# Kernel tuning notes

Measured on AMD Instinct MI355X. Metric: run time of the kernel, lower is better.

## Reference

```python
import jax, jax.numpy as jnp
import numpy as np

N = 100000
D = 128
E = 3200000

def setup_inputs() -> dict:
    key = jax.random.key(0)
    k1, k2, k3 = jax.random.split(key, 3)
    mu = jax.random.normal(k1, (N, D), dtype=jnp.float32)
    log_sigma = jax.random.normal(k2, (N, D), dtype=jnp.float32)
    edge_index = jax.random.randint(k3, (2, E), 0, N, dtype=jnp.int64)
    return {"mu": mu, "log_sigma": log_sigma, "edge_index": edge_index}

def reference(mu, log_sigma, edge_index):
    # elbo() for variational_distribution='Gaussian'
    sigma = jnp.exp(log_sigma)
    # likelihood: gather endpoints, squared L2 distance, log(sigmoid(-d2))
    diff = mu[edge_index[0]] - mu[edge_index[1]]        # [E, D]
    d2 = jnp.sum(diff * diff, axis=1)                    # [E]
    log_likelihood = jnp.sum(jax.nn.log_sigmoid(-d2))    # log(sigmoid(-d2)), stable
    # Gaussian KL to standard normal prior
    kl = 0.5 * jnp.sum(sigma * sigma + mu * mu - log_sigma - 1.0)
    return -log_likelihood + kl
```

## Files before the change

### kernel.cpp

```cpp
#include <hip/hip_runtime.h>


#define NN 100000
#define DD 128
#define NBI 8
#define NBJ 16
#define NBINS 128
#define BSI 12500
#define BSJ 6250

#define NKL 512
#define NSCA 1024
#define SLICEA 32u
#define CAPA 32768u
#define OCAP 131072u
#define LOVF 768
#define SENT 0xFFFFFFFFu

#define QSCALE 21.166666f
#define S2Q    0.0022320293f

#define CAPB 26624u
#define NKLB 512
#define NSCB 1536

typedef unsigned int uint_t;
typedef float floatx2 __attribute__((ext_vector_type(2)));

#define WA_OCURS  64
#define WA_OFLOW  1024
#define WA_MU8    (WA_OFLOW + 1048576)
#define WA_PAIRS  (WA_MU8 + 12800000)
#define WA_END    (WA_PAIRS + 16777216)

#define WB_CURSOR 256
#define WB_MU8    16384
#define WB_PAIRS  (WB_MU8 + 12800000)
#define PAIRB_BYTES (NBINS * (int)CAPB * 4)
#define WB_END    (WB_PAIRS + PAIRB_BYTES)

__device__ inline double block_reduce_add(double v) {
    for (int off = 32; off > 0; off >>= 1)
        v += __shfl_down(v, off, 64);
    __shared__ double lds[8];
    int wid  = threadIdx.x >> 6;
    int lane = threadIdx.x & 63;
    if (lane == 0) lds[wid] = v;
    __syncthreads();
    double r = 0.0;
    if (threadIdx.x == 0) {
        int nw = (blockDim.x + 63) >> 6;
        for (int w = 0; w < nw; ++w) r += lds[w];
    }
    return r;
}

__device__ inline double edge_term(float d2) {
    double t = (double)d2;
    if (d2 < 30.0f) t += (double)log1pf(expf(-d2));
    return t;
}

__device__ inline float d2_fp32(const float* __restrict__ mu, int i, int j) {
    const float* pa = mu + (size_t)i * DD;
    const float* pb = mu + (size_t)j * DD;
    float d2 = 0.0f;
    for (int d = 0; d < DD; ++d) {
        float df = pa[d] - pb[d];
        d2 += df * df;
    }
    return d2;
}

__device__ inline int dot4acc(unsigned int a, unsigned int b, int acc) {
#if __has_builtin(__builtin_amdgcn_sdot4)
    return __builtin_amdgcn_sdot4((int)a, (int)b, acc, false);
#else
    int s = acc;
    #pragma unroll
    for (int t = 0; t < 4; ++t) {
        int xa = (int)((a >> (8 * t)) & 0xFFu); xa = (xa ^ 0x80) - 0x80;
        int xb = (int)((b >> (8 * t)) & 0xFFu); xb = (xb ^ 0x80) - 0x80;
        s += xa * xb;
    }
    return s;
#endif
}

__device__ inline int d2_int_part(uint4 a, uint4 b) {
    int daa = 0, dbb = 0, dab = 0;
    daa = dot4acc(a.x, a.x, daa); daa = dot4acc(a.y, a.y, daa);
    daa = dot4acc(a.z, a.z, daa); daa = dot4acc(a.w, a.w, daa);
    dbb = dot4acc(b.x, b.x, dbb); dbb = dot4acc(b.y, b.y, dbb);
    dbb = dot4acc(b.z, b.z, dbb); dbb = dot4acc(b.w, b.w, dbb);
    dab = dot4acc(a.x, b.x, dab); dab = dot4acc(a.y, b.y, dab);
    dab = dot4acc(a.z, b.z, dab); dab = dot4acc(a.w, b.w, dab);
    return daa + dbb - 2 * dab;
}

__device__ inline float d2_part(uint4 a, uint4 b) {
    float p = 0.0f;
    const unsigned int* pa = &a.x;
    const unsigned int* pb = &b.x;
    #pragma unroll
    for (int k = 0; k < 4; ++k) {
        floatx2 a0 = __builtin_amdgcn_cvt_pk_f32_fp8(pa[k], false);
        floatx2 a1 = __builtin_amdgcn_cvt_pk_f32_fp8(pa[k], true);
        floatx2 b0 = __builtin_amdgcn_cvt_pk_f32_fp8(pb[k], false);
        floatx2 b1 = __builtin_amdgcn_cvt_pk_f32_fp8(pb[k], true);
        float d0 = a0.x - b0.x;
        float d1 = a0.y - b0.y;
        float d2 = a1.x - b1.x;
        float d3 = a1.y - b1.y;
        p += d0 * d0 + d1 * d1 + d2 * d2 + d3 * d3;
    }
    return p;
}

__global__ void front_kernel(const float* __restrict__ mu,
                             const float* __restrict__ ls,
                             unsigned int* __restrict__ mu8,
                             const int* __restrict__ ei,
                             uint_t* __restrict__ pairs,
                             uint2* __restrict__ oflow,
                             uint_t* __restrict__ ocurs,
                             double* __restrict__ ws,
                             int total4, int E, int chunk) {
    __shared__ uint_t lcnt[NBINS];
    __shared__ uint_t stage[NBINS * (int)SLICEA];
    __shared__ uint2  lovf[LOVF];
    __shared__ uint_t lovfc;
    __shared__ uint_t obase;
    double acc = 0.0;
    if (blockIdx.x < NKL) {
        int stride = NKL * blockDim.x;
        for (int i = blockIdx.x * blockDim.x + threadIdx.x; i < total4; i += stride) {
            float4 m = reinterpret_cast<const float4*>(mu)[i];
            float4 s = reinterpret_cast<const float4*>(ls)[i];
            float v;
            v  = 0.5f * (expf(2.0f * s.x) + m.x * m.x - s.x - 1.0f);
            v += 0.5f * (expf(2.0f * s.y) + m.y * m.y - s.y - 1.0f);
            v += 0.5f * (expf(2.0f * s.z) + m.z * m.z - s.z - 1.0f);
            v += 0.5f * (expf(2.0f * s.w) + m.w * m.w - s.w - 1.0f);
            acc += (double)v;
            int q0 = __float2int_rn(fminf(fmaxf(m.x * QSCALE, -127.f), 127.f));
            int q1 = __float2int_rn(fminf(fmaxf(m.y * QSCALE, -127.f), 127.f));
            int q2 = __float2int_rn(fminf(fmaxf(m.z * QSCALE, -127.f), 127.f));
            int q3 = __float2int_rn(fminf(fmaxf(m.w * QSCALE, -127.f), 127.f));
            unsigned int pk = (unsigned int)(q0 & 255) |
                              ((unsigned int)(q1 & 255) << 8) |
                              ((unsigned int)(q2 & 255) << 16) |
                              ((unsigned int)(q3 & 255) << 24);
            mu8[i] = pk;
        }
    } else {
        int b = blockIdx.x - NKL;
        int t = threadIdx.x;
        for (int k = t; k < NBINS; k += blockDim.x) lcnt[k] = 0u;
        for (int k = t; k < NBINS * (int)SLICEA; k += blockDim.x) stage[k] = SENT;
        if (t == 0) lovfc = 0u;
        __syncthreads();
        int s = b * chunk, tend = min(E, s + chunk);
        for (int e = s + t; e < tend; e += blockDim.x) {
            int i = min(max(ei[e], 0), NN - 1);
            int j = min(max(ei[E + e], 0), NN - 1);
            int bi = i / BSI, bj = j / BSJ;
            int bin = bi * NBJ + bj;
            uint_t r = atomicAdd(&lcnt[bin], 1u);
            if (r < SLICEA) {
                stage[bin * (int)SLICEA + (int)r] =
                    ((uint_t)(i - bi * BSI) << 17) | (uint_t)j;
            } else {
                uint_t ro = atomicAdd(&lovfc, 1u);
                if (ro < LOVF) {
                    lovf[ro] = make_uint2((uint_t)i, (uint_t)j);
                } else {
                    acc += edge_term(d2_fp32(mu, i, j));
                }
            }
        }
        __syncthreads();
        for (int idx = t; idx < NBINS * (int)SLICEA; idx += blockDim.x) {
            int bin = idx >> 5, r = idx & 31;
            pairs[(size_t)bin * CAPA + (uint_t)b * SLICEA + (uint_t)r] = stage[idx];
        }
        uint_t nov = min(lovfc, (uint_t)LOVF);
        if (t == 0 && nov) obase = atomicAdd(ocurs, nov);
        __syncthreads();
        if (nov) {
            uint_t bo = obase;
            for (uint_t o = t; o < nov; o += blockDim.x) {
                if (bo + o < OCAP) {
                    oflow[bo + o] = lovf[o];
                } else {
                    uint2 pr = lovf[o];
                    acc += edge_term(d2_fp32(mu, (int)pr.x, (int)pr.y));
                }
            }
        }
    }
    double r = block_reduce_add(acc);
    if (threadIdx.x == 0) atomicAdd(ws, r);
}

__global__ void ll_sortedA_kernel(const unsigned int* __restrict__ mu8,
                                  const uint_t* __restrict__ pairs,
                                  const uint2* __restrict__ oflow,
                                  const uint_t* __restrict__ ocurs,
                                  double* __restrict__ ws) {
    int xcd  = blockIdx.x & 7;
    int lane = threadIdx.x & 7;
    unsigned int g  = (blockIdx.x >> 3) * (blockDim.x >> 3) + (threadIdx.x >> 3);
    unsigned int GP = (gridDim.x >> 3) * (blockDim.x >> 3);
    unsigned int gl = blockIdx.x * (blockDim.x >> 3) + (threadIdx.x >> 3);
    unsigned int GT = gridDim.x * (blockDim.x >> 3);
    unsigned int s    = (unsigned int)xcd * (NBJ * CAPA);
    unsigned int tend = s + NBJ * CAPA;
    unsigned int ibase = (unsigned int)(xcd * BSI);
    const uint4* tb = reinterpret_cast<const uint4*>(mu8);
    double acc = 0.0;
    for (unsigned int e0 = s + g; e0 < tend; e0 += 4u * GP) {
        unsigned int e1 = e0 + GP;
        unsigned int e2 = e0 + 2u * GP;
        unsigned int e3 = e0 + 3u * GP;
        uint_t p0 = pairs[e0];
        uint_t p1 = (e1 < tend) ? pairs[e1] : SENT;
        uint_t p2 = (e2 < tend) ? pairs[e2] : SENT;
        uint_t p3 = (e3 < tend) ? pairs[e3] : SENT;
        unsigned int i0 = min(ibase + (p0 >> 17), (unsigned int)(NN - 1));
        unsigned int j0 = min(p0 & 131071u,       (unsigned int)(NN - 1));
        unsigned int i1 = min(ibase + (p1 >> 17), (unsigned int)(NN - 1));
        unsigned int j1 = min(p1 & 131071u,       (unsigned int)(NN - 1));
        unsigned int i2 = min(ibase + (p2 >> 17), (unsigned int)(NN - 1));
        unsigned int j2 = min(p2 & 131071u,       (unsigned int)(NN - 1));
        unsigned int i3 = min(ibase + (p3 >> 17), (unsigned int)(NN - 1));
        unsigned int j3 = min(p3 & 131071u,       (unsigned int)(NN - 1));
        uint4 a0 = tb[(size_t)i0 * 8 + lane];
        uint4 b0 = tb[(size_t)j0 * 8 + lane];
        uint4 a1 = tb[(size_t)i1 * 8 + lane];
        uint4 b1 = tb[(size_t)j1 * 8 + lane];
        uint4 a2 = tb[(size_t)i2 * 8 + lane];
        uint4 b2 = tb[(size_t)j2 * 8 + lane];
        uint4 a3 = tb[(size_t)i3 * 8 + lane];
        uint4 b3 = tb[(size_t)j3 * 8 + lane];
        int d0 = d2_int_part(a0, b0);
        int d1 = d2_int_part(a1, b1);
        int d2 = d2_int_part(a2, b2);
        int d3 = d2_int_part(a3, b3);
        #pragma unroll
        for (int m = 4; m >= 1; m >>= 1) {
            d0 += __shfl_xor(d0, m, 64);
            d1 += __shfl_xor(d1, m, 64);
            d2 += __shfl_xor(d2, m, 64);
            d3 += __shfl_xor(d3, m, 64);
        }
        if (lane == 0) {
            if (!(p0 & 0x80000000u)) acc += edge_term(S2Q * (float)d0);
            if (!(p1 & 0x80000000u)) acc += edge_term(S2Q * (float)d1);
            if (!(p2 & 0x80000000u)) acc += edge_term(S2Q * (float)d2);
            if (!(p3 & 0x80000000u)) acc += edge_term(S2Q * (float)d3);
        }
    }
    unsigned int oc = min(*ocurs, OCAP);
    for (unsigned int o = gl; o < oc; o += GT) {
        uint2 pr = oflow[o];
        unsigned int i = min(pr.x, (unsigned int)(NN - 1));
        unsigned int j = min(pr.y, (unsigned int)(NN - 1));
        uint4 a = tb[(size_t)i * 8 + lane];
        uint4 b = tb[(size_t)j * 8 + lane];
        int d = d2_int_part(a, b);
        #pragma unroll
        for (int m = 4; m >= 1; m >>= 1)
            d += __shfl_xor(d, m, 64);
        if (lane == 0) acc += edge_term(S2Q * (float)d);
    }
    double r = block_reduce_add(acc);
    if (threadIdx.x == 0) atomicAdd(ws, r);
}

__global__ void frontB_kernel(const float* __restrict__ mu,
                              const float* __restrict__ ls,
                              unsigned int* __restrict__ mu8,
                              const int* __restrict__ ei,
                              uint_t* __restrict__ pairs,
                              uint_t* __restrict__ cursor,
                              double* __restrict__ ws,
                              int total4, int E, int chunk) {
    __shared__ uint_t lh[NBINS];
    __shared__ uint_t lb[NBINS];
    double acc = 0.0;
    if (blockIdx.x < NKLB) {
        int stride = NKLB * blockDim.x;
        for (int i = blockIdx.x * blockDim.x + threadIdx.x; i < total4; i += stride) {
            float4 m = reinterpret_cast<const float4*>(mu)[i];
            float4 s = reinterpret_cast<const float4*>(ls)[i];
            float v;
            v  = 0.5f * (expf(2.0f * s.x) + m.x * m.x - s.x - 1.0f);
            v += 0.5f * (expf(2.0f * s.y) + m.y * m.y - s.y - 1.0f);
            v += 0.5f * (expf(2.0f * s.z) + m.z * m.z - s.z - 1.0f);
            v += 0.5f * (expf(2.0f * s.w) + m.w * m.w - s.w - 1.0f);
            acc += (double)v;
            int w = __builtin_amdgcn_cvt_pk_fp8_f32(m.x, m.y, 0, false);
            w     = __builtin_amdgcn_cvt_pk_fp8_f32(m.z, m.w, w, true);
            mu8[i] = (unsigned int)w;
        }
    } else {
        int b = blockIdx.x - NKLB;
        int t = threadIdx.x;
        for (int k = t; k < NBINS; k += blockDim.x) lh[k] = 0u;
        __syncthreads();
        int s = b * chunk, tend = min(E, s + chunk);
        for (int e = s + t; e < tend; e += blockDim.x) {
            int i = min(max(ei[e], 0), NN - 1);
            int j = min(max(ei[E + e], 0), NN - 1);
            atomicAdd(&lh[(i / BSI) * NBJ + j / BSJ], 1u);
        }
        __syncthreads();
        if (t < NBINS) lb[t] = atomicAdd(&cursor[t << 4], lh[t]);
        __syncthreads();
        if (t < NBINS) lh[t] = lb[t];
        __syncthreads();
        for (int e = s + t; e < tend; e += blockDim.x) {
            int i = min(max(ei[e], 0), NN - 1);
            int j = min(max(ei[E + e], 0), NN - 1);
            int bi = i / BSI, bj = j / BSJ;
            int bin = bi * NBJ + bj;
            uint_t r = atomicAdd(&lh[bin], 1u);
            if (r < CAPB) {
                pairs[(size_t)bin * CAPB + r] =
                    ((uint_t)(i - bi * BSI) << 17) | (uint_t)j;
            } else {
                acc += edge_term(d2_fp32(mu, i, j));
            }
        }
    }
    double r = block_reduce_add(acc);
    if (threadIdx.x == 0) atomicAdd(ws, r);
}

__global__ void ll_sortedB_kernel(const unsigned int* __restrict__ mu8,
                                  const uint_t* __restrict__ pairs,
                                  const uint_t* __restrict__ cursor,
                                  double* __restrict__ ws) {
    int xcd  = blockIdx.x & 7;
    int lane = threadIdx.x & 7;
    unsigned int g  = (blockIdx.x >> 3) * (blockDim.x >> 3) + (threadIdx.x >> 3);
    unsigned int GP = (gridDim.x >> 3) * (blockDim.x >> 3);
    unsigned int s    = (unsigned int)xcd * (NBJ * CAPB);
    unsigned int tend = s + NBJ * CAPB;
    unsigned int ibase = (unsigned int)(xcd * BSI);
    const uint4* tb = reinterpret_cast<const uint4*>(mu8);
    double acc = 0.0;
    for (unsigned int e0 = s + g; e0 < tend; e0 += 2u * GP) {
        unsigned int e1 = e0 + GP;
        unsigned int bin0 = e0 / CAPB, r0 = e0 - bin0 * CAPB;
        unsigned int bin1 = e1 / CAPB, r1 = e1 - bin1 * CAPB;
        unsigned int c0 = min(cursor[bin0 << 4], CAPB);
        bool v0 = r0 < c0;
        bool v1 = (e1 < tend) && (r1 < min(cursor[bin1 << 4], CAPB));
        if (v0) {
            uint_t p0 = pairs[e0];
            unsigned int i0 = min(ibase + (p0 >> 17), (unsigned int)(NN - 1));
            unsigned int j0 = min(p0 & 131071u,       (unsigned int)(NN - 1));
            uint4 a0 = tb[(size_t)i0 * 8 + lane];
            uint4 b0 = tb[(size_t)j0 * 8 + lane];
            float q0 = d2_part(a0, b0);
            #pragma unroll
            for (int m = 4; m >= 1; m >>= 1)
                q0 += __shfl_xor(q0, m, 64);
            if (lane == 0) acc += edge_term(q0);
        }
        if (v1) {
            uint_t p1 = pairs[e1];
            unsigned int i1 = min(ibase + (p1 >> 17), (unsigned int)(NN - 1));
            unsigned int j1 = min(p1 & 131071u,       (unsigned int)(NN - 1));
            uint4 a1 = tb[(size_t)i1 * 8 + lane];
            uint4 b1 = tb[(size_t)j1 * 8 + lane];
            float q1 = d2_part(a1, b1);
            #pragma unroll
            for (int m = 4; m >= 1; m >>= 1)
                q1 += __shfl_xor(q1, m, 64);
            if (lane == 0) acc += edge_term(q1);
        }
    }
    double r = block_reduce_add(acc);
    if (threadIdx.x == 0) atomicAdd(ws, r);
}

__global__ void kl_conv_kernel(const float* __restrict__ mu,
                               const float* __restrict__ ls,
                               unsigned int* __restrict__ mu8,
                               double* __restrict__ ws, int total4) {
    int stride = gridDim.x * blockDim.x;
    double acc = 0.0;
    for (int i = blockIdx.x * blockDim.x + threadIdx.x; i < total4; i += stride) {
        float4 m = reinterpret_cast<const float4*>(mu)[i];
        float4 s = reinterpret_cast<const float4*>(ls)[i];
        float v;
        v  = 0.5f * (expf(2.0f * s.x) + m.x * m.x - s.x - 1.0f);
        v += 0.5f * (expf(2.0f * s.y) + m.y * m.y - s.y - 1.0f);
        v += 0.5f * (expf(2.0f * s.z) + m.z * m.z - s.z - 1.0f);
        v += 0.5f * (expf(2.0f * s.w) + m.w * m.w - s.w - 1.0f);
        acc += (double)v;
        if (mu8) {
            int w = __builtin_amdgcn_cvt_pk_fp8_f32(m.x, m.y, 0, false);
            w     = __builtin_amdgcn_cvt_pk_fp8_f32(m.z, m.w, w, true);
            mu8[i] = (unsigned int)w;
        }
    }
    double r = block_reduce_add(acc);
    if (threadIdx.x == 0) atomicAdd(ws, r);
}

__global__ void ll8_kernel(const unsigned int* __restrict__ mu8,
                           const int* __restrict__ ei,
                           double* __restrict__ ws, int E) {
    int gid     = (blockIdx.x * blockDim.x + threadIdx.x) >> 3;
    int lane    = threadIdx.x & 7;
    int ngroups = (gridDim.x * blockDim.x) >> 3;
    double acc = 0.0;
    const uint4* base = reinterpret_cast<const uint4*>(mu8);
    for (int e = gid; e < E; e += 2 * ngroups) {
        int e1 = e + ngroups;
        bool has2 = e1 < E;
        int i0 = min(max(ei[e], 0), NN - 1);
        int j0 = min(max(ei[E + e], 0), NN - 1);
        int i1 = has2 ? min(max(ei[e1], 0), NN - 1) : i0;
        int j1 = has2 ? min(max(ei[E + e1], 0), NN - 1) : j0;
        uint4 a0 = base[(size_t)i0 * 8 + lane];
        uint4 b0 = base[(size_t)j0 * 8 + lane];
        uint4 a1 = base[(size_t)i1 * 8 + lane];
        uint4 b1 = base[(size_t)j1 * 8 + lane];
        float p0 = d2_part(a0, b0);
        float p1 = d2_part(a1, b1);
        #pragma unroll
        for (int m = 4; m >= 1; m >>= 1) {
            p0 += __shfl_xor(p0, m, 64);
            p1 += __shfl_xor(p1, m, 64);
        }
        if (lane == 0) {
            acc += edge_term(p0);
            if (has2) acc += edge_term(p1);
        }
    }
    double r = block_reduce_add(acc);
    if (threadIdx.x == 0) atomicAdd(ws, r);
}

__global__ void ll32_kernel(const float* __restrict__ mu,
                            const int* __restrict__ ei,
                            double* __restrict__ ws, int E) {
    int gid     = (blockIdx.x * blockDim.x + threadIdx.x) >> 5;
    int lane    = threadIdx.x & 31;
    int ngroups = (gridDim.x * blockDim.x) >> 5;
    double acc = 0.0;
    for (int e = gid; e < E; e += ngroups) {
        int i = min(max(ei[e], 0), NN - 1);
        int j = min(max(ei[E + e], 0), NN - 1);
        const float4* a = reinterpret_cast<const float4*>(mu + (size_t)i * DD);
        const float4* b = reinterpret_cast<const float4*>(mu + (size_t)j * DD);
        float4 av = a[lane];
        float4 bv = b[lane];
        float dx = av.x - bv.x;
        float dy = av.y - bv.y;
        float dz = av.z - bv.z;
        float dw = av.w - bv.w;
        float p = dx * dx + dy * dy + dz * dz + dw * dw;
        for (int m = 16; m >= 1; m >>= 1)
            p += __shfl_xor(p, m, 64);
        if (lane == 0)
            acc += edge_term(p);
    }
    double r = block_reduce_add(acc);
    if (threadIdx.x == 0) atomicAdd(ws, r);
}

__global__ void init_kernel(double* ws, float* out) {
    if (threadIdx.x == 0) { ws[0] = 0.0; out[0] = 0.0f; }
}

__global__ void finalize_kernel(const double* __restrict__ ws,
                                float* __restrict__ out) {
    if (blockIdx.x == 0 && threadIdx.x == 0)
        out[0] = (float)ws[0];
}

extern "C" void kernel_launch(void* const* d_in, const int* in_sizes, int n_in,
                              void* d_out, int out_size, void* d_ws, size_t ws_size,
                              hipStream_t stream) {
    const float* mu = (const float*)d_in[0];
    const float* ls = (const float*)d_in[1];
    const int*   ei = (const int*)d_in[2];
    float* out = (float*)d_out;
    char*  wsb = (char*)d_ws;
    double* ws = (double*)d_ws;

    const int E = in_sizes[2] / 2;
    const int total4 = (NN * DD) / 4;

    if (ws_size >= (size_t)WA_END) {
        uint_t* ocurs = reinterpret_cast<uint_t*>(wsb + WA_OCURS);
        uint2*  oflow = reinterpret_cast<uint2*>(wsb + WA_OFLOW);
        unsigned int* mu8 = reinterpret_cast<unsigned int*>(wsb + WA_MU8);
        uint_t* pairs = reinterpret_cast<uint_t*>(wsb + WA_PAIRS);
        const int chunk = (E + NSCA - 1) / NSCA;

        hipMemsetAsync(wsb, 0, 1024, stream);
        front_kernel<<<NKL + NSCA, 256, 0, stream>>>(mu, ls, mu8, ei, pairs,
                                                     oflow, ocurs, ws,
                                                     total4, E, chunk);
        ll_sortedA_kernel<<<2048, 256, 0, stream>>>(mu8, pairs, oflow, ocurs, ws);
    } else if (ws_size >= (size_t)WB_END) {
        uint_t* cursor = reinterpret_cast<uint_t*>(wsb + WB_CURSOR);
        unsigned int* mu8 = reinterpret_cast<unsigned int*>(wsb + WB_MU8);
        uint_t* pairs = reinterpret_cast<uint_t*>(wsb + WB_PAIRS);
        const int chunk = (E + NSCB - 1) / NSCB;

        hipMemsetAsync(wsb, 0, 16384, stream);
        frontB_kernel<<<NKLB + NSCB, 256, 0, stream>>>(mu, ls, mu8, ei, pairs,
                                                       cursor, ws, total4, E, chunk);
        ll_sortedB_kernel<<<2048, 256, 0, stream>>>(mu8, pairs, cursor, ws);
    } else {
        const bool use_fp8 = (ws_size >= (size_t)WB_MU8 + 12800000u);
        unsigned int* mu8 = use_fp8
            ? reinterpret_cast<unsigned int*>(wsb + WB_MU8) : nullptr;
        init_kernel<<<1, 64, 0, stream>>>(ws, out);
        kl_conv_kernel<<<1024, 256, 0, stream>>>(mu, ls, mu8, ws, total4);
        if (use_fp8)
            ll8_kernel<<<2048, 256, 0, stream>>>(mu8, ei, ws, E);
        else
            ll32_kernel<<<2048, 256, 0, stream>>>(mu, ei, ws, E);
    }
    finalize_kernel<<<1, 64, 0, stream>>>(ws, out);
}
```

Baseline: 106.2 us.

## Record per-slice bin counts and skip sentinel padding in sorted edge pass

The front kernel now writes each scatter block's per-bin fill count to a new count array and no longer prefills the LDS staging buffer with sentinels. The likelihood kernel walks (bin, block) slices and loops only over the valid entries in each slice, so it no longer loads gathers for padding slots. The number of KL/quantize blocks is also doubled. The price is variable-length inner loops with clamped duplicate loads and an extra count array read.

```diff
diff --git a/kernel.cpp b/kernel.cpp
--- a/kernel.cpp
+++ b/kernel.cpp
@@ -9,7 +9,7 @@
 #define BSI 12500
 #define BSJ 6250
 
-#define NKL 512
+#define NKL 1024
 #define NSCA 1024
 #define SLICEA 32u
 #define CAPA 32768u
@@ -28,7 +28,8 @@
 typedef float floatx2 __attribute__((ext_vector_type(2)));
 
 #define WA_OCURS  64
-#define WA_OFLOW  1024
+#define WA_CNT    1024
+#define WA_OFLOW  (WA_CNT + 524288)
 #define WA_MU8    (WA_OFLOW + 1048576)
 #define WA_PAIRS  (WA_MU8 + 12800000)
 #define WA_END    (WA_PAIRS + 16777216)
@@ -122,6 +123,7 @@
                              unsigned int* __restrict__ mu8,
                              const int* __restrict__ ei,
                              uint_t* __restrict__ pairs,
+                             uint_t* __restrict__ cnt,
                              uint2* __restrict__ oflow,
                              uint_t* __restrict__ ocurs,
                              double* __restrict__ ws,
@@ -157,7 +159,6 @@
         int b = blockIdx.x - NKL;
         int t = threadIdx.x;
         for (int k = t; k < NBINS; k += blockDim.x) lcnt[k] = 0u;
-        for (int k = t; k < NBINS * (int)SLICEA; k += blockDim.x) stage[k] = SENT;
         if (t == 0) lovfc = 0u;
         __syncthreads();
         int s = b * chunk, tend = min(E, s + chunk);
@@ -184,6 +185,8 @@
             int bin = idx >> 5, r = idx & 31;
             pairs[(size_t)bin * CAPA + (uint_t)b * SLICEA + (uint_t)r] = stage[idx];
         }
+        for (int k = t; k < NBINS; k += blockDim.x)
+            cnt[b * NBINS + k] = min(lcnt[k], SLICEA);
         uint_t nov = min(lovfc, (uint_t)LOVF);
         if (t == 0 && nov) obase = atomicAdd(ocurs, nov);
         __syncthreads();
@@ -205,60 +208,67 @@
 
 __global__ void ll_sortedA_kernel(const unsigned int* __restrict__ mu8,
                                   const uint_t* __restrict__ pairs,
+                                  const uint_t* __restrict__ cnt,
                                   const uint2* __restrict__ oflow,
                                   const uint_t* __restrict__ ocurs,
                                   double* __restrict__ ws) {
     int xcd  = blockIdx.x & 7;
     int lane = threadIdx.x & 7;
     unsigned int g  = (blockIdx.x >> 3) * (blockDim.x >> 3) + (threadIdx.x >> 3);
-    unsigned int GP = (gridDim.x >> 3) * (blockDim.x >> 3);
+    unsigned int NG = (gridDim.x >> 3) * (blockDim.x >> 3);
     unsigned int gl = blockIdx.x * (blockDim.x >> 3) + (threadIdx.x >> 3);
     unsigned int GT = gridDim.x * (blockDim.x >> 3);
-    unsigned int s    = (unsigned int)xcd * (NBJ * CAPA);
-    unsigned int tend = s + NBJ * CAPA;
     unsigned int ibase = (unsigned int)(xcd * BSI);
     const uint4* tb = reinterpret_cast<const uint4*>(mu8);
-    double acc = 0.0;
-    for (unsigned int e0 = s + g; e0 < tend; e0 += 4u * GP) {
-        unsigned int e1 = e0 + GP;
-        unsigned int e2 = e0 + 2u * GP;
-        unsigned int e3 = e0 + 3u * GP;
-        uint_t p0 = pairs[e0];
-        uint_t p1 = (e1 < tend) ? pairs[e1] : SENT;
-        uint_t p2 = (e2 < tend) ? pairs[e2] : SENT;
-        uint_t p3 = (e3 < tend) ? pairs[e3] : SENT;
-        unsigned int i0 = min(ibase + (p0 >> 17), (unsigned int)(NN - 1));
-        unsigned int j0 = min(p0 & 131071u,       (unsigned int)(NN - 1));
-        unsigned int i1 = min(ibase + (p1 >> 17), (unsigned int)(NN - 1));
-        unsigned int j1 = min(p1 & 131071u,       (unsigned int)(NN - 1));
-        unsigned int i2 = min(ibase + (p2 >> 17), (unsigned int)(NN - 1));
-        unsigned int j2 = min(p2 & 131071u,       (unsigned int)(NN - 1));
-        unsigned int i3 = min(ibase + (p3 >> 17), (unsigned int)(NN - 1));
-        unsigned int j3 = min(p3 & 131071u,       (unsigned int)(NN - 1));
-        uint4 a0 = tb[(size_t)i0 * 8 + lane];
-        uint4 b0 = tb[(size_t)j0 * 8 + lane];
-        uint4 a1 = tb[(size_t)i1 * 8 + lane];
-        uint4 b1 = tb[(size_t)j1 * 8 + lane];
-        uint4 a2 = tb[(size_t)i2 * 8 + lane];
-        uint4 b2 = tb[(size_t)j2 * 8 + lane];
-        uint4 a3 = tb[(size_t)i3 * 8 + lane];
-        uint4 b3 = tb[(size_t)j3 * 8 + lane];
-        int d0 = d2_int_part(a0, b0);
-        int d1 = d2_int_part(a1, b1);
-        int d2 = d2_int_part(a2, b2);
-        int d3 = d2_int_part(a3, b3);
-        #pragma unroll
-        for (int m = 4; m >= 1; m >>= 1) {
-            d0 += __shfl_xor(d0, m, 64);
-            d1 += __shfl_xor(d1, m, 64);
-            d2 += __shfl_xor(d2, m, 64);
-            d3 += __shfl_xor(d3, m, 64);
-        }
-        if (lane == 0) {
-            if (!(p0 & 0x80000000u)) acc += edge_term(S2Q * (float)d0);
-            if (!(p1 & 0x80000000u)) acc += edge_term(S2Q * (float)d1);
-            if (!(p2 & 0x80000000u)) acc += edge_term(S2Q * (float)d2);
-            if (!(p3 & 0x80000000u)) acc += edge_term(S2Q * (float)d3);
+    const unsigned int SLICES = NBJ * NSCA;
+    double acc = 0.0;
+    for (unsigned int sl = g; sl < SLICES; sl += NG) {
+        unsigned int bj  = sl >> 10;
+        unsigned int blk = sl & (NSCA - 1);
+        unsigned int bin = (unsigned int)xcd * NBJ + bj;
+        unsigned int cv = min(cnt[blk * NBINS + bin], SLICEA);
+        const uint_t* sp = pairs + (size_t)bin * CAPA + (size_t)blk * SLICEA;
+        for (unsigned int r = 0; r < cv; r += 4) {
+            unsigned int r1 = min(r + 1u, cv - 1u);
+            unsigned int r2 = min(r + 2u, cv - 1u);
+            unsigned int r3 = min(r + 3u, cv - 1u);
+            uint_t p0 = sp[r];
+            uint_t p1 = sp[r1];
+            uint_t p2 = sp[r2];
+            uint_t p3 = sp[r3];
+            unsigned int i0 = min(ibase + (p0 >> 17), (unsigned int)(NN - 1));
+            unsigned int j0 = min(p0 & 131071u,       (unsigned int)(NN - 1));
+            unsigned int i1 = min(ibase + (p1 >> 17), (unsigned int)(NN - 1));
+            unsigned int j1 = min(p1 & 131071u,       (unsigned int)(NN - 1));
+            unsigned int i2 = min(ibase + (p2 >> 17), (unsigned int)(NN - 1));
+            unsigned int j2 = min(p2 & 131071u,       (unsigned int)(NN - 1));
+            unsigned int i3 = min(ibase + (p3 >> 17), (unsigned int)(NN - 1));
+            unsigned int j3 = min(p3 & 131071u,       (unsigned int)(NN - 1));
+            uint4 a0 = tb[(size_t)i0 * 8 + lane];
+            uint4 b0 = tb[(size_t)j0 * 8 + lane];
+            uint4 a1 = tb[(size_t)i1 * 8 + lane];
+            uint4 b1 = tb[(size_t)j1 * 8 + lane];
+            uint4 a2 = tb[(size_t)i2 * 8 + lane];
+            uint4 b2 = tb[(size_t)j2 * 8 + lane];
+            uint4 a3 = tb[(size_t)i3 * 8 + lane];
+            uint4 b3 = tb[(size_t)j3 * 8 + lane];
+            int d0 = d2_int_part(a0, b0);
+            int d1 = d2_int_part(a1, b1);
+            int d2 = d2_int_part(a2, b2);
+            int d3 = d2_int_part(a3, b3);
+            #pragma unroll
+            for (int m = 4; m >= 1; m >>= 1) {
+                d0 += __shfl_xor(d0, m, 64);
+                d1 += __shfl_xor(d1, m, 64);
+                d2 += __shfl_xor(d2, m, 64);
+                d3 += __shfl_xor(d3, m, 64);
+            }
+            if (lane == 0) {
+                acc += edge_term(S2Q * (float)d0);
+                if (r + 1u < cv) acc += edge_term(S2Q * (float)d1);
+                if (r + 2u < cv) acc += edge_term(S2Q * (float)d2);
+                if (r + 3u < cv) acc += edge_term(S2Q * (float)d3);
+            }
         }
     }
     unsigned int oc = min(*ocurs, OCAP);
@@ -500,6 +510,7 @@
 
     if (ws_size >= (size_t)WA_END) {
         uint_t* ocurs = reinterpret_cast<uint_t*>(wsb + WA_OCURS);
+        uint_t* cnt   = reinterpret_cast<uint_t*>(wsb + WA_CNT);
         uint2*  oflow = reinterpret_cast<uint2*>(wsb + WA_OFLOW);
         unsigned int* mu8 = reinterpret_cast<unsigned int*>(wsb + WA_MU8);
         uint_t* pairs = reinterpret_cast<uint_t*>(wsb + WA_PAIRS);
@@ -507,9 +518,10 @@
 
         hipMemsetAsync(wsb, 0, 1024, stream);
         front_kernel<<<NKL + NSCA, 256, 0, stream>>>(mu, ls, mu8, ei, pairs,
-                                                     oflow, ocurs, ws,
+                                                     cnt, oflow, ocurs, ws,
                                                      total4, E, chunk);
-        ll_sortedA_kernel<<<2048, 256, 0, stream>>>(mu8, pairs, oflow, ocurs, ws);
+        ll_sortedA_kernel<<<2048, 256, 0, stream>>>(mu8, pairs, cnt,
+                                                    oflow, ocurs, ws);
     } else if (ws_size >= (size_t)WB_END) {
         uint_t* cursor = reinterpret_cast<uint_t*>(wsb + WB_CURSOR);
         unsigned int* mu8 = reinterpret_cast<unsigned int*>(wsb + WB_MU8);
```

Result: slower. 115.1 us (+8.4%).
